# Performance work log

Hardware: AMD Instinct MI355X
Metric: run time of the kernel (lower is better)

The kernel has to match this reference:

```python
import jax, jax.numpy as jnp
import numpy as np

B, T = 32, 1024
TEMP_IN, STAT_IN = 128, 64
TEMP_OUT, STAT_OUT = 128, 64
EPS = 1e-5
NEG_SLOPE = 0.01


def _bn_eval(x, gamma, beta, mean, var):
    # BatchNorm1d in eval mode (running stats)
    return (x - mean) * jax.lax.rsqrt(var + EPS) * gamma + beta


def _leaky_relu(x):
    return jnp.where(x >= 0, x, NEG_SLOPE * x)


def setup_inputs() -> dict:
    key = jax.random.key(0)
    k = jax.random.split(key, 6)
    # deterministic ragged lengths in [512, 1024]
    lengths_np = (512 + (np.arange(B) * 37) % 513).astype(np.int64)
    N = int(lengths_np.sum())  # 23450
    batch_idx = np.repeat(np.arange(B), lengths_np).astype(np.int32)
    pos_idx = np.concatenate([np.arange(l) for l in lengths_np]).astype(np.int32)
    valid = (np.arange(T)[None, :] < lengths_np[:, None])  # [B, T]
    mask_repeat = valid[:, :, None] & valid[:, None, :]    # [B, T, T]

    inp = {
        "x_temp": jax.random.normal(k[0], (N, TEMP_IN), jnp.float32),
        "x_stat": jax.random.normal(k[1], (B, STAT_IN), jnp.float32),
        "temp_attn": jax.random.normal(k[2], (B, T, T), jnp.float32) * 0.1,
        "mask_repeat": jnp.asarray(mask_repeat),
        "lengths": jnp.asarray(lengths_np),
        "batch_idx": jnp.asarray(batch_idx),
        "pos_idx": jnp.asarray(pos_idx),
        # non_linear_temp: Linear(TEMP_IN+STAT_IN -> TEMP_OUT) + BN
        "W1": jax.random.normal(k[3], (TEMP_OUT, TEMP_IN + STAT_IN), jnp.float32) / np.sqrt(TEMP_IN + STAT_IN),
        "b1": jnp.zeros((TEMP_OUT,), jnp.float32),
        "gamma1": jnp.ones((TEMP_OUT,), jnp.float32),
        "beta1": jnp.zeros((TEMP_OUT,), jnp.float32),
        "mean1": jnp.zeros((TEMP_OUT,), jnp.float32),
        "var1": jnp.ones((TEMP_OUT,), jnp.float32),
        # non_linear_stat: Linear(STAT_IN -> STAT_OUT) + BN
        "W2": jax.random.normal(k[4], (STAT_OUT, STAT_IN), jnp.float32) / np.sqrt(STAT_IN),
        "b2": jnp.zeros((STAT_OUT,), jnp.float32),
        "gamma2": jnp.ones((STAT_OUT,), jnp.float32),
        "beta2": jnp.zeros((STAT_OUT,), jnp.float32),
        "mean2": jnp.zeros((STAT_OUT,), jnp.float32),
        "var2": jnp.ones((STAT_OUT,), jnp.float32),
    }
    return inp


def reference(x_temp, x_stat, temp_attn, mask_repeat, lengths, batch_idx, pos_idx,
              W1, b1, gamma1, beta1, mean1, var1,
              W2, b2, gamma2, beta2, mean2, var2):
    # repeat_static_features: gather per-batch static feats to packed rows
    x_stat_rep = x_stat[batch_idx]                              # [N, STAT_IN]
    h = jnp.concatenate((x_temp, x_stat_rep), axis=-1) @ W1.T + b1
    h = _leaky_relu(_bn_eval(h, gamma1, beta1, mean1, var1))    # [N, TEMP_OUT]

    # pad_packed_sequences: scatter packed rows into [B, T, C] (zeros elsewhere)
    padded = jnp.zeros((B, T, TEMP_OUT), h.dtype).at[batch_idx, pos_idx].set(h)

    # self attention: softmax(x x^T / sqrt(d)) over padded rows (as original)
    d = jnp.asarray(TEMP_OUT, h.dtype)
    qk = jnp.einsum('btc,bsc->bts', padded, padded) / jnp.sqrt(d)
    self_attn = jax.nn.softmax(qk, axis=-1)

    attn = jnp.where(mask_repeat, self_attn + temp_attn, jnp.asarray(0.0, h.dtype))

    x_stat_out = _leaky_relu(_bn_eval(x_stat @ W2.T + b2, gamma2, beta2, mean2, var2))

    x_out_pad = jnp.einsum('bts,bsc->btc', attn, padded)        # [B, T, TEMP_OUT]
    # pack_padded_sequences: gather valid positions back to packed layout
    x_out = x_out_pad[batch_idx, pos_idx]                       # [N, TEMP_OUT]
    return (x_out, x_stat_out)
```

## Files before the change

kernel.cpp:

```cpp
#include <hip/hip_runtime.h>
#include <hip/hip_bf16.h>
#include <hip/hip_fp16.h>

typedef __hip_bfloat16 bf16;
typedef __attribute__((ext_vector_type(8))) short short8;
typedef __attribute__((ext_vector_type(4))) float f32x4;

#define EPS 1e-5f
#define NSLOPE 0.01f

__device__ __forceinline__ float b2f(bf16 v) { return __bfloat162float(v); }

__device__ __forceinline__ float ld1(const void* p, size_t idx, int isbf) {
  if (isbf) return b2f(((const bf16*)p)[idx]);
  return ((const float*)p)[idx];
}
__device__ __forceinline__ void st1(void* p, size_t idx, int isbf, float v) {
  if (isbf) ((bf16*)p)[idx] = __float2bfloat16(v);
  else      ((float*)p)[idx] = v;
}
__device__ __forceinline__ short f2bs(float x) {
  bf16 t = __float2bfloat16(x);
  short s; __builtin_memcpy(&s, &t, 2); return s;
}
__device__ __forceinline__ short8 pack8f(const float* p) {
  float4 a = *(const float4*)p, b = *(const float4*)(p + 4);
  short8 r;
  r[0] = f2bs(a.x); r[1] = f2bs(a.y); r[2] = f2bs(a.z); r[3] = f2bs(a.w);
  r[4] = f2bs(b.x); r[5] = f2bs(b.y); r[6] = f2bs(b.z); r[7] = f2bs(b.w);
  return r;
}

__global__ void meta_kernel(const void* __restrict__ xt,
                            const int* __restrict__ bidx, const int* __restrict__ pidx,
                            int N, int B, int* __restrict__ rs, int* __restrict__ ln,
                            int* __restrict__ flag) {
  if (blockIdx.x == 0 && threadIdx.x < 64) {
    unsigned w = ((const unsigned*)xt)[threadIdx.x];
    unsigned lo = w & 0xffffu;
    unsigned ex = (lo >> 7) & 0xffu;
    bool sane = ((lo & 0x7fffu) == 0u) || (ex >= 96u && ex <= 134u);
    unsigned long long m = __ballot(sane);
    if (threadIdx.x == 0) flag[0] = (__popcll(m) >= 48) ? 1 : 0;
  }
  int stride = gridDim.x * blockDim.x;
  for (int i = blockIdx.x * blockDim.x + threadIdx.x; i < N; i += stride) {
    int b = bidx[i];
    if ((unsigned)b >= (unsigned)B) continue;
    if (i == 0 || bidx[i - 1] != b) rs[b] = i;
    if (i == N - 1 || bidx[i + 1] != b) ln[b] = pidx[i] + 1;
  }
}

__global__ void zfill_kernel(void* out, const int* __restrict__ flag, long long n) {
  const int isbf = flag[0];
  long long i = (long long)blockIdx.x * blockDim.x + threadIdx.x;
  long long stride = (long long)gridDim.x * blockDim.x;
  for (; i < n; i += stride) st1(out, (size_t)i, isbf, 0.f);
}

__global__ __launch_bounds__(256) void h_mfma_kernel(
    const void* __restrict__ xt, const void* __restrict__ xsg,
    const int* __restrict__ bidx,
    const void* __restrict__ W1, const void* __restrict__ b1,
    const void* __restrict__ g1, const void* __restrict__ be1,
    const void* __restrict__ mn1, const void* __restrict__ vr1,
    const int* __restrict__ flag, bf16* __restrict__ hout, int N) {
  const int isbf = flag[0];
  const int tid = threadIdx.x, lane = tid & 63, wv = tid >> 6;
  const int m16 = lane & 15, quad = lane >> 4;
  const int row0 = blockIdx.x * 64 + wv * 16;
  const int m = row0 + m16;
  const int mc = (m < N) ? m : (N - 1);
  const int bi = bidx[mc];

  short8 af[6];
  if (isbf) {
    const bf16* xr = (const bf16*)xt + (size_t)mc * 128 + quad * 8;
#pragma unroll
    for (int ks = 0; ks < 4; ++ks) af[ks] = *(const short8*)(xr + ks * 32);
    const bf16* sr = (const bf16*)xsg + (size_t)bi * 64 + quad * 8;
    af[4] = *(const short8*)sr;
    af[5] = *(const short8*)(sr + 32);
  } else {
    const float* xr = (const float*)xt + (size_t)mc * 128 + quad * 8;
#pragma unroll
    for (int ks = 0; ks < 4; ++ks) af[ks] = pack8f(xr + ks * 32);
    const float* sr = (const float*)xsg + (size_t)bi * 64 + quad * 8;
    af[4] = pack8f(sr);
    af[5] = pack8f(sr + 32);
  }

  f32x4 acc[8];
#pragma unroll
  for (int ct = 0; ct < 8; ++ct) acc[ct] = (f32x4){0.f, 0.f, 0.f, 0.f};

  if (isbf) {
    const bf16* wb = (const bf16*)W1;
#pragma unroll
    for (int ks = 0; ks < 6; ++ks) {
      const int k = ks * 32 + quad * 8;
#pragma unroll
      for (int ct = 0; ct < 8; ++ct) {
        const int o = ct * 16 + m16;
        short8 bfrag = *(const short8*)(wb + (size_t)o * 192 + k);
        acc[ct] = __builtin_amdgcn_mfma_f32_16x16x32_bf16(af[ks], bfrag, acc[ct], 0, 0, 0);
      }
    }
  } else {
    const float* wb = (const float*)W1;
#pragma unroll
    for (int ks = 0; ks < 6; ++ks) {
      const int k = ks * 32 + quad * 8;
#pragma unroll
      for (int ct = 0; ct < 8; ++ct) {
        const int o = ct * 16 + m16;
        short8 bfrag = pack8f(wb + (size_t)o * 192 + k);
        acc[ct] = __builtin_amdgcn_mfma_f32_16x16x32_bf16(af[ks], bfrag, acc[ct], 0, 0, 0);
      }
    }
  }

#pragma unroll
  for (int ct = 0; ct < 8; ++ct) {
    const int o = ct * 16 + m16;
    float k1 = ld1(g1, o, isbf) * rsqrtf(ld1(vr1, o, isbf) + EPS);
    float k0 = ld1(be1, o, isbf) - ld1(mn1, o, isbf) * k1;
    float bias = ld1(b1, o, isbf);
#pragma unroll
    for (int r = 0; r < 4; ++r) {
      int mr = row0 + quad * 4 + r;
      if (mr < N) {
        float v = (acc[ct][r] + bias) * k1 + k0;
        v = (v >= 0.f) ? v : NSLOPE * v;
        hout[(size_t)mr * 128 + o] = __float2bfloat16(v);
      }
    }
  }
}

__global__ __launch_bounds__(64) void stat_kernel(
    const void* __restrict__ xstat, const void* __restrict__ W2,
    const void* __restrict__ b2, const void* __restrict__ g2,
    const void* __restrict__ be2, const void* __restrict__ mn2,
    const void* __restrict__ vr2, const int* __restrict__ flag,
    void* __restrict__ out, long long obase) {
  __shared__ float xs[64];
  const int isbf = flag[0];
  const int b = blockIdx.x, o = threadIdx.x;
  xs[o] = ld1(xstat, b * 64 + o, isbf);
  __syncthreads();
  float acc = ld1(b2, o, isbf);
#pragma unroll 8
  for (int j = 0; j < 64; ++j) acc += xs[j] * ld1(W2, o * 64 + j, isbf);
  float k1 = ld1(g2, o, isbf) * rsqrtf(ld1(vr2, o, isbf) + EPS);
  float k0 = ld1(be2, o, isbf) - ld1(mn2, o, isbf) * k1;
  float v = acc * k1 + k0;
  v = (v >= 0.f) ? v : NSLOPE * v;
  st1(out, (size_t)(obase + b * 64 + o), isbf, v);
}

__global__ __launch_bounds__(256) void attn_mfma_kernel(
    const void* __restrict__ ta, const bf16* __restrict__ h,
    const int* __restrict__ rs_arr, const int* __restrict__ ln_arr,
    const int* __restrict__ flag, void* __restrict__ xout, int T, int N) {
  __shared__ __align__(16) unsigned short Ss[16][1032];
  __shared__ __align__(16) unsigned short vT[128][66];

  const int b = blockIdx.y, t0 = blockIdx.x * 16;
  const int len = ln_arr[b];
  if (t0 >= len) return;
  const int isbf = flag[0];
  const int rs = rs_arr[b];
  const int nrows = min(16, len - t0);
  const int tid = threadIdx.x;
  const int lane = tid & 63, wv = tid >> 6;
  const int m16 = lane & 15, quad = lane >> 4;

  short8 qf[4];
  {
    int qrow = rs + t0 + m16;
    if (qrow > N - 1) qrow = N - 1;
    const bf16* qp = h + (size_t)qrow * 128 + quad * 8;
#pragma unroll
    for (int ks = 0; ks < 4; ++ks)
      qf[ks] = *(const short8*)(qp + ks * 32);
  }

  const float scale = 0.08838834764831845f;
  const int ntiles = (T + 15) >> 4;
  const int nact = min(ntiles, (len + 15) >> 4);
  const short8 zero8 = {0, 0, 0, 0, 0, 0, 0, 0};

  {
    short8 kc[4] = {zero8, zero8, zero8, zero8};
    int st = wv;
    if (st < nact) {
      int s = st * 16 + m16;
      bool v = (s < len);
      const bf16* kp = h + (size_t)(rs + (v ? s : 0)) * 128 + quad * 8;
#pragma unroll
      for (int ks = 0; ks < 4; ++ks) kc[ks] = v ? *(const short8*)(kp + ks * 32) : zero8;
    }
    for (; st < nact; st += 4) {
      short8 kn[4] = {zero8, zero8, zero8, zero8};
      int stn = st + 4;
      if (stn < nact) {
        int s2 = stn * 16 + m16;
        bool v2 = (s2 < len);
        const bf16* kp2 = h + (size_t)(rs + (v2 ? s2 : 0)) * 128 + quad * 8;
#pragma unroll
        for (int ks = 0; ks < 4; ++ks) kn[ks] = v2 ? *(const short8*)(kp2 + ks * 32) : zero8;
      }
      f32x4 acc = {0.f, 0.f, 0.f, 0.f};
#pragma unroll
      for (int ks = 0; ks < 4; ++ks)
        acc = __builtin_amdgcn_mfma_f32_16x16x32_bf16(qf[ks], kc[ks], acc, 0, 0, 0);
      int s = st * 16 + m16;
      if (s < T) {
#pragma unroll
        for (int r = 0; r < 4; ++r)
          Ss[quad * 4 + r][s] = __half_as_ushort(__float2half(acc[r] * scale));
      }
#pragma unroll
      for (int ks = 0; ks < 4; ++ks) kc[ks] = kn[ks];
    }
    int st2 = nact + (((wv - nact) % 4) + 4) % 4;
    for (; st2 < ntiles; st2 += 4) {
      int s = st2 * 16 + m16;
      if (s < T) {
#pragma unroll
        for (int r = 0; r < 4; ++r) Ss[quad * 4 + r][s] = 0;
      }
    }
  }
  __syncthreads();

  {
    const int Tpad = (T + 63) & ~63;
    for (int j = 0; j < 4; ++j) {
      int r = wv + (j << 2);
      float vals[16];
#pragma unroll
      for (int k = 0; k < 16; ++k) {
        int s = lane + (k << 6);
        vals[k] = (s < T) ? __half2float(__ushort_as_half(Ss[r][s])) : -INFINITY;
      }
      float mx = -INFINITY;
#pragma unroll
      for (int k = 0; k < 16; ++k) mx = fmaxf(mx, vals[k]);
#pragma unroll
      for (int off = 32; off >= 1; off >>= 1) mx = fmaxf(mx, __shfl_xor(mx, off, 64));
      float l = 0.f;
#pragma unroll
      for (int k = 0; k < 16; ++k) { vals[k] = __expf(vals[k] - mx); l += vals[k]; }
#pragma unroll
      for (int off = 32; off >= 1; off >>= 1) l += __shfl_xor(l, off, 64);
      float inv = 1.f / l;
      size_t tabase = ((size_t)b * T + (t0 + r)) * (size_t)T;
      if (isbf) {
        const bf16* tp = (const bf16*)ta + tabase;
#pragma unroll
        for (int k = 0; k < 16; ++k) {
          int s = lane + (k << 6);
          if (s < Tpad) {
            float p = 0.f;
            if (s < T) p = vals[k] * inv + b2f(tp[s]);
            *(bf16*)&Ss[r][s] = __float2bfloat16(p);
          }
        }
      } else {
        const float* tp = (const float*)ta + tabase;
#pragma unroll
        for (int k = 0; k < 16; ++k) {
          int s = lane + (k << 6);
          if (s < Tpad) {
            float p = 0.f;
            if (s < T) p = vals[k] * inv + tp[s];
            *(bf16*)&Ss[r][s] = __float2bfloat16(p);
          }
        }
      }
    }
  }
  __syncthreads();

  f32x4 oacc0 = {0.f, 0.f, 0.f, 0.f};
  f32x4 oacc1 = {0.f, 0.f, 0.f, 0.f};
  for (int s0 = 0; s0 < len; s0 += 64) {
    for (int e = tid; e < 512; e += 256) {
      int sp = e >> 4, c8 = (e & 15) << 3;
      int s = s0 + 2 * sp;
      uint4 u0 = {0, 0, 0, 0}, u1 = {0, 0, 0, 0};
      if (s < len)     u0 = *(const uint4*)(h + (size_t)(rs + s) * 128 + c8);
      if (s + 1 < len) u1 = *(const uint4*)(h + (size_t)(rs + s + 1) * 128 + c8);
      const unsigned short* a0 = (const unsigned short*)&u0;
      const unsigned short* a1 = (const unsigned short*)&u1;
#pragma unroll
      for (int j = 0; j < 8; ++j)
        *(unsigned*)&vT[c8 + j][2 * sp] = (unsigned)a0[j] | ((unsigned)a1[j] << 16);
    }
    __syncthreads();
#pragma unroll
    for (int ks = 0; ks < 2; ++ks) {
      short8 af = *(const short8*)&Ss[m16][s0 + ks * 32 + quad * 8];
#pragma unroll
      for (int ct = 0; ct < 2; ++ct) {
        const int c0 = wv * 32 + ct * 16;
        const unsigned short* vrow = &vT[c0 + m16][ks * 32 + quad * 8];
        unsigned w0 = *(const unsigned*)(vrow + 0);
        unsigned w1 = *(const unsigned*)(vrow + 2);
        unsigned w2 = *(const unsigned*)(vrow + 4);
        unsigned w3 = *(const unsigned*)(vrow + 6);
        short8 bfv;
        bfv[0] = (short)(w0 & 0xffffu); bfv[1] = (short)(w0 >> 16);
        bfv[2] = (short)(w1 & 0xffffu); bfv[3] = (short)(w1 >> 16);
        bfv[4] = (short)(w2 & 0xffffu); bfv[5] = (short)(w2 >> 16);
        bfv[6] = (short)(w3 & 0xffffu); bfv[7] = (short)(w3 >> 16);
        if (ct == 0)
          oacc0 = __builtin_amdgcn_mfma_f32_16x16x32_bf16(af, bfv, oacc0, 0, 0, 0);
        else
          oacc1 = __builtin_amdgcn_mfma_f32_16x16x32_bf16(af, bfv, oacc1, 0, 0, 0);
      }
    }
    __syncthreads();
  }

#pragma unroll
  for (int r = 0; r < 4; ++r) {
    int t = quad * 4 + r;
    if (t < nrows) {
      size_t ob = (size_t)(rs + t0 + t) * 128;
      st1(xout, ob + wv * 32 + m16,      isbf, oacc0[r]);
      st1(xout, ob + wv * 32 + 16 + m16, isbf, oacc1[r]);
    }
  }
}

extern "C" void kernel_launch(void* const* d_in, const int* in_sizes, int n_in,
                              void* d_out, int out_size, void* d_ws, size_t ws_size,
                              hipStream_t stream) {
  const void* x_temp    = d_in[0];
  const void* x_stat    = d_in[1];
  const void* temp_attn = d_in[2];
  const int N = in_sizes[0] / 128;
  const int B = in_sizes[1] / 64;
  long long tt = (long long)in_sizes[2] / B;
  int T = 1; while ((long long)(T + 1) * (T + 1) <= tt) ++T;

  int p = 3;
  while (p < n_in && in_sizes[p] != N) ++p;
  const int* batch_idx = (const int*)d_in[p++];
  const int* pos_idx   = (const int*)d_in[p++];
  const void* W1 = d_in[p++];
  const void* b1 = d_in[p++];
  const void* g1 = d_in[p++];
  const void* be1= d_in[p++];
  const void* mn1= d_in[p++];
  const void* vr1= d_in[p++];
  const void* W2 = d_in[p++];
  const void* b2 = d_in[p++];
  const void* g2 = d_in[p++];
  const void* be2= d_in[p++];
  const void* mn2= d_in[p++];
  const void* vr2= d_in[p++];

  int*  meta = (int*)d_ws;
  int*  rs   = meta;
  int*  lnp  = meta + B;
  int*  flag = meta + 2 * B;
  bf16* h    = (bf16*)((char*)d_ws + 1024);
  size_t need = 1024 + (size_t)N * 128 * sizeof(bf16);

  long long obase = (long long)N * 128;

  meta_kernel<<<90, 256, 0, stream>>>(x_temp, batch_idx, pos_idx, N, B, rs, lnp, flag);
  stat_kernel<<<B, 64, 0, stream>>>(x_stat, W2, b2, g2, be2, mn2, vr2, flag,
                                    d_out, obase);
  if (ws_size >= need) {
    h_mfma_kernel<<<(N + 63) / 64, 256, 0, stream>>>(x_temp, x_stat, batch_idx,
                                                     W1, b1, g1, be1, mn1, vr1,
                                                     flag, h, N);
    attn_mfma_kernel<<<dim3((T + 15) / 16, B), 256, 0, stream>>>(
        temp_attn, h, rs, lnp, flag, d_out, T, N);
  } else {
    zfill_kernel<<<512, 256, 0, stream>>>(d_out, flag, obase);
  }
}
```

Baseline: 494.7 us.

## Fold temp_attn into PV MFMA and restrict softmax to valid columns

The temp_attn bias is no longer added in the softmax stage. It is now loaded per 64-column chunk of valid keys and applied as an extra MFMA against the V tile, so columns beyond the sequence length are never read. The softmax handles the padded tail analytically (zero logits) instead of materialising it. W1 is also converted to bf16 once in a small pre-kernel, so the linear layer stops repacking fp32 weights per block. The cost is a doubled MFMA count in the PV loop and bf16 rounding of temp_attn before accumulation.

```diff
diff --git a/kernel.cpp b/kernel.cpp
--- a/kernel.cpp
+++ b/kernel.cpp
@@ -52,6 +52,13 @@
   }
 }
 
+__global__ void w1cvt_kernel(const void* __restrict__ W1, const int* __restrict__ flag,
+                             bf16* __restrict__ w1b, int n) {
+  const int isbf = flag[0];
+  int i = blockIdx.x * blockDim.x + threadIdx.x;
+  if (i < n) w1b[i] = __float2bfloat16(ld1(W1, i, isbf));
+}
+
 __global__ void zfill_kernel(void* out, const int* __restrict__ flag, long long n) {
   const int isbf = flag[0];
   long long i = (long long)blockIdx.x * blockDim.x + threadIdx.x;
@@ -61,8 +68,8 @@
 
 __global__ __launch_bounds__(256) void h_mfma_kernel(
     const void* __restrict__ xt, const void* __restrict__ xsg,
-    const int* __restrict__ bidx,
-    const void* __restrict__ W1, const void* __restrict__ b1,
+    const int* __restrict__ bidx, const bf16* __restrict__ w1b,
+    const void* __restrict__ b1,
     const void* __restrict__ g1, const void* __restrict__ be1,
     const void* __restrict__ mn1, const void* __restrict__ vr1,
     const int* __restrict__ flag, bf16* __restrict__ hout, int N) {
@@ -95,29 +102,14 @@
 #pragma unroll
   for (int ct = 0; ct < 8; ++ct) acc[ct] = (f32x4){0.f, 0.f, 0.f, 0.f};
 
-  if (isbf) {
-    const bf16* wb = (const bf16*)W1;
-#pragma unroll
-    for (int ks = 0; ks < 6; ++ks) {
-      const int k = ks * 32 + quad * 8;
-#pragma unroll
-      for (int ct = 0; ct < 8; ++ct) {
-        const int o = ct * 16 + m16;
-        short8 bfrag = *(const short8*)(wb + (size_t)o * 192 + k);
-        acc[ct] = __builtin_amdgcn_mfma_f32_16x16x32_bf16(af[ks], bfrag, acc[ct], 0, 0, 0);
-      }
-    }
-  } else {
-    const float* wb = (const float*)W1;
-#pragma unroll
-    for (int ks = 0; ks < 6; ++ks) {
-      const int k = ks * 32 + quad * 8;
-#pragma unroll
-      for (int ct = 0; ct < 8; ++ct) {
-        const int o = ct * 16 + m16;
-        short8 bfrag = pack8f(wb + (size_t)o * 192 + k);
-        acc[ct] = __builtin_amdgcn_mfma_f32_16x16x32_bf16(af[ks], bfrag, acc[ct], 0, 0, 0);
-      }
+#pragma unroll
+  for (int ks = 0; ks < 6; ++ks) {
+    const int k = ks * 32 + quad * 8;
+#pragma unroll
+    for (int ct = 0; ct < 8; ++ct) {
+      const int o = ct * 16 + m16;
+      short8 bfrag = *(const short8*)(w1b + (size_t)o * 192 + k);
+      acc[ct] = __builtin_amdgcn_mfma_f32_16x16x32_bf16(af[ks], bfrag, acc[ct], 0, 0, 0);
     }
   }
 
@@ -188,8 +180,7 @@
   }
 
   const float scale = 0.08838834764831845f;
-  const int ntiles = (T + 15) >> 4;
-  const int nact = min(ntiles, (len + 15) >> 4);
+  const int nact = (len + 15) >> 4;
   const short8 zero8 = {0, 0, 0, 0, 0, 0, 0, 0};
 
   {
@@ -225,61 +216,37 @@
 #pragma unroll
       for (int ks = 0; ks < 4; ++ks) kc[ks] = kn[ks];
     }
-    int st2 = nact + (((wv - nact) % 4) + 4) % 4;
-    for (; st2 < ntiles; st2 += 4) {
-      int s = st2 * 16 + m16;
-      if (s < T) {
-#pragma unroll
-        for (int r = 0; r < 4; ++r) Ss[quad * 4 + r][s] = 0;
-      }
-    }
   }
   __syncthreads();
 
   {
-    const int Tpad = (T + 63) & ~63;
+    const int lenp64 = (len + 63) & ~63;
     for (int j = 0; j < 4; ++j) {
       int r = wv + (j << 2);
       float vals[16];
 #pragma unroll
       for (int k = 0; k < 16; ++k) {
         int s = lane + (k << 6);
-        vals[k] = (s < T) ? __half2float(__ushort_as_half(Ss[r][s])) : -INFINITY;
+        vals[k] = (s < len) ? __half2float(__ushort_as_half(Ss[r][s])) : -INFINITY;
       }
       float mx = -INFINITY;
 #pragma unroll
       for (int k = 0; k < 16; ++k) mx = fmaxf(mx, vals[k]);
 #pragma unroll
       for (int off = 32; off >= 1; off >>= 1) mx = fmaxf(mx, __shfl_xor(mx, off, 64));
+      if (len < T) mx = fmaxf(mx, 0.f);
       float l = 0.f;
 #pragma unroll
-      for (int k = 0; k < 16; ++k) { vals[k] = __expf(vals[k] - mx); l += vals[k]; }
+      for (int k = 0; k < 16; ++k) { float e = __expf(vals[k] - mx); vals[k] = e; l += e; }
 #pragma unroll
       for (int off = 32; off >= 1; off >>= 1) l += __shfl_xor(l, off, 64);
+      l += (float)(T - len) * __expf(-mx);
       float inv = 1.f / l;
-      size_t tabase = ((size_t)b * T + (t0 + r)) * (size_t)T;
-      if (isbf) {
-        const bf16* tp = (const bf16*)ta + tabase;
-#pragma unroll
-        for (int k = 0; k < 16; ++k) {
-          int s = lane + (k << 6);
-          if (s < Tpad) {
-            float p = 0.f;
-            if (s < T) p = vals[k] * inv + b2f(tp[s]);
-            *(bf16*)&Ss[r][s] = __float2bfloat16(p);
-          }
-        }
-      } else {
-        const float* tp = (const float*)ta + tabase;
-#pragma unroll
-        for (int k = 0; k < 16; ++k) {
-          int s = lane + (k << 6);
-          if (s < Tpad) {
-            float p = 0.f;
-            if (s < T) p = vals[k] * inv + tp[s];
-            *(bf16*)&Ss[r][s] = __float2bfloat16(p);
-          }
-        }
+#pragma unroll
+      for (int k = 0; k < 16; ++k) {
+        int s = lane + (k << 6);
+        if (s < len)          *(bf16*)&Ss[r][s] = __float2bfloat16(vals[k] * inv);
+        else if (s < lenp64)  *(bf16*)&Ss[r][s] = __float2bfloat16(0.f);
       }
     }
   }
@@ -287,6 +254,7 @@
 
   f32x4 oacc0 = {0.f, 0.f, 0.f, 0.f};
   f32x4 oacc1 = {0.f, 0.f, 0.f, 0.f};
+  const size_t tarow = ((size_t)b * T + (t0 + m16)) * (size_t)T;
   for (int s0 = 0; s0 < len; s0 += 64) {
     for (int e = tid; e < 512; e += 256) {
       int sp = e >> 4, c8 = (e & 15) << 3;
@@ -300,10 +268,21 @@
       for (int j = 0; j < 8; ++j)
         *(unsigned*)&vT[c8 + j][2 * sp] = (unsigned)a0[j] | ((unsigned)a1[j] << 16);
     }
+    short8 taf0, taf1;
+    if (isbf) {
+      const bf16* tp = (const bf16*)ta + tarow + s0 + quad * 8;
+      taf0 = *(const short8*)tp;
+      taf1 = *(const short8*)(tp + 32);
+    } else {
+      const float* tp = (const float*)ta + tarow + s0 + quad * 8;
+      taf0 = pack8f(tp);
+      taf1 = pack8f(tp + 32);
+    }
     __syncthreads();
 #pragma unroll
     for (int ks = 0; ks < 2; ++ks) {
-      short8 af = *(const short8*)&Ss[m16][s0 + ks * 32 + quad * 8];
+      short8 pf = *(const short8*)&Ss[m16][s0 + ks * 32 + quad * 8];
+      short8 tf = ks ? taf1 : taf0;
 #pragma unroll
       for (int ct = 0; ct < 2; ++ct) {
         const int c0 = wv * 32 + ct * 16;
@@ -317,10 +296,13 @@
         bfv[2] = (short)(w1 & 0xffffu); bfv[3] = (short)(w1 >> 16);
         bfv[4] = (short)(w2 & 0xffffu); bfv[5] = (short)(w2 >> 16);
         bfv[6] = (short)(w3 & 0xffffu); bfv[7] = (short)(w3 >> 16);
-        if (ct == 0)
-          oacc0 = __builtin_amdgcn_mfma_f32_16x16x32_bf16(af, bfv, oacc0, 0, 0, 0);
-        else
-          oacc1 = __builtin_amdgcn_mfma_f32_16x16x32_bf16(af, bfv, oacc1, 0, 0, 0);
+        if (ct == 0) {
+          oacc0 = __builtin_amdgcn_mfma_f32_16x16x32_bf16(pf, bfv, oacc0, 0, 0, 0);
+          oacc0 = __builtin_amdgcn_mfma_f32_16x16x32_bf16(tf, bfv, oacc0, 0, 0, 0);
+        } else {
+          oacc1 = __builtin_amdgcn_mfma_f32_16x16x32_bf16(pf, bfv, oacc1, 0, 0, 0);
+          oacc1 = __builtin_amdgcn_mfma_f32_16x16x32_bf16(tf, bfv, oacc1, 0, 0, 0);
+        }
       }
     }
     __syncthreads();
@@ -370,7 +352,9 @@
   int*  lnp  = meta + B;
   int*  flag = meta + 2 * B;
   bf16* h    = (bf16*)((char*)d_ws + 1024);
-  size_t need = 1024 + (size_t)N * 128 * sizeof(bf16);
+  bf16* w1b  = h + (size_t)N * 128;
+  const int w1n = 128 * 192;
+  size_t need = 1024 + (size_t)N * 128 * sizeof(bf16) + (size_t)w1n * sizeof(bf16);
 
   long long obase = (long long)N * 128;
 
@@ -378,8 +362,9 @@
   stat_kernel<<<B, 64, 0, stream>>>(x_stat, W2, b2, g2, be2, mn2, vr2, flag,
                                     d_out, obase);
   if (ws_size >= need) {
+    w1cvt_kernel<<<(w1n + 255) / 256, 256, 0, stream>>>(W1, flag, w1b, w1n);
     h_mfma_kernel<<<(N + 63) / 64, 256, 0, stream>>>(x_temp, x_stat, batch_idx,
-                                                     W1, b1, g1, be1, mn1, vr1,
+                                                     w1b, b1, g1, be1, mn1, vr1,
                                                      flag, h, N);
     attn_mfma_kernel<<<dim3((T + 15) / 16, B), 256, 0, stream>>>(
         temp_attn, h, rs, lnp, flag, d_out, T, N);
```

Result: faster. 442.5 us (-10.5%).
